# Kernel optimization log

Hardware: AMD Instinct MI355X
Metric: run time of the kernel (lower is better)

The kernel has to match this reference:

```python
import jax, jax.numpy as jnp
import numpy as np

B, T, C, HS = 256, 256, 384, 64


def setup_inputs() -> dict:
    key = jax.random.key(0)
    k1, k2, k3, k4 = jax.random.split(key, 4)
    X = jax.random.normal(k1, (B, T, C), dtype=jnp.float32)
    Wq = jax.random.normal(k2, (C, HS), dtype=jnp.float32) * (C ** -0.5)
    Wk = jax.random.normal(k3, (C, HS), dtype=jnp.float32) * (C ** -0.5)
    Wv = jax.random.normal(k4, (C, HS), dtype=jnp.float32) * (C ** -0.5)
    return {"X": X, "Wq": Wq, "Wk": Wk, "Wv": Wv}


def reference(X, Wq, Wk, Wv):
    # Single causal self-attention head (dropout in eval mode / identity).
    num_channels = X.shape[-1]
    q = jnp.einsum('btc,ch->bth', X, Wq)  # [B,T,HS]
    k = jnp.einsum('btc,ch->bth', X, Wk)
    v = jnp.einsum('btc,ch->bth', X, Wv)
    # NOTE: original scales by embedding dim C**-0.5, not head_size**-0.5.
    scores = jnp.einsum('bqh,bkh->bqk', q, k) * (num_channels ** -0.5)  # [B,T,T]
    Tq = X.shape[1]
    causal = jnp.tril(jnp.ones((Tq, Tq), dtype=bool))
    scores = jnp.where(causal, scores, jnp.float32(-jnp.inf))
    weights = jax.nn.softmax(scores, axis=-1)
    return jnp.einsum('bqk,bkh->bqh', weights, v)  # [B,T,HS]
```

## Files before the change

kernel.cpp:

```cpp
#include <hip/hip_runtime.h>
#include <hip/hip_bf16.h>

#define B_  256
#define T_  256
#define C_  384
#define HS_ 64
#define BT_ (B_*T_)

typedef __attribute__((ext_vector_type(8))) short short8;
typedef __attribute__((ext_vector_type(4))) float f32x4;

__device__ __forceinline__ unsigned short f2bf(float f) {
    unsigned u = __float_as_uint(f);
    u += 0x7FFFu + ((u >> 16) & 1u);
    return (unsigned short)(u >> 16);
}

__global__ __launch_bounds__(256) void prep_wfrag(
    const float* __restrict__ Wq, const float* __restrict__ Wk,
    const float* __restrict__ Wv, unsigned short* __restrict__ Wfrag)
{
    const int tid  = blockIdx.x * 256 + threadIdx.x;
    const int lane = tid & 63;
    const int q    = tid >> 6;
    const int f    = q % 3;
    const int q2   = q / 3;
    const int wn   = q2 & 3;
    const int s    = q2 >> 2;

    const int n     = wn * 48 + f * 16 + (lane & 15);
    const int kbase = s * 32 + (lane >> 4) * 8;
    const float* src = (n < 64) ? Wq : (n < 128) ? Wk : Wv;
    const int c      = n & 63;
    const float scale = (n < 64) ? 0.05103103630798288f : 1.0f;

    short8 out;
    #pragma unroll
    for (int j = 0; j < 8; ++j)
        out[j] = (short)f2bf(src[(size_t)(kbase + j) * HS_ + c] * scale);
    *(short8*)&Wfrag[(size_t)tid * 8] = out;
}

#define LQ_OFF 0
#define LK_OFF 18432
#define LV_OFF 36864
#define LX_OFF 53760

__global__ __launch_bounds__(1024, 4) void head_fused(
    const float* __restrict__ X, const unsigned short* __restrict__ Wfrag,
    float* __restrict__ out)
{
    __shared__ unsigned short lds[74240];
    const int t    = threadIdx.x;
    const int w    = t >> 6;
    const int lane = t & 63;
    const int lo   = lane & 15;
    const int hi   = lane >> 4;
    const int b    = blockIdx.x;
    const int wm   = w >> 2, wn = w & 3;

    const float* Xb = X + (size_t)b * T_ * C_;
    const short8* Wf = (const short8*)Wfrag;

    const int srow  = t >> 2;
    const int squad = t & 3;

    auto stage_load = [&](int k0, float4* g) {
        const float* p = Xb + (size_t)srow * C_ + k0 + squad * 8;
        g[0] = *(const float4*)(p);
        g[1] = *(const float4*)(p + 4);
    };
    auto stage_write = [&](int buf, const float4* g) {
        short8 p;
        p[0] = (short)f2bf(g[0].x); p[1] = (short)f2bf(g[0].y);
        p[2] = (short)f2bf(g[0].z); p[3] = (short)f2bf(g[0].w);
        p[4] = (short)f2bf(g[1].x); p[5] = (short)f2bf(g[1].y);
        p[6] = (short)f2bf(g[1].z); p[7] = (short)f2bf(g[1].w);
        *(short8*)&lds[LX_OFF + buf * 10240 + srow * 40 + squad * 8] = p;
    };
    auto load_w = [&](int s, short8* wf) {
        const short8* base = Wf + ((size_t)(s * 4 + wn) * 3) * 64 + lane;
        #pragma unroll
        for (int f = 0; f < 3; ++f)
            wf[f] = base[f * 64];
    };

    float4 gx[2][2];
    short8 wfr[2][3];
    stage_load(0, gx[0]);
    load_w(0, wfr[0]);
    stage_load(32, gx[1]);
    stage_write(0, gx[0]);
    __syncthreads();

    f32x4 acc[4][3];
    #pragma unroll
    for (int m = 0; m < 4; ++m)
        #pragma unroll
        for (int f = 0; f < 3; ++f)
            acc[m][f] = (f32x4){0.f, 0.f, 0.f, 0.f};

    #pragma unroll 2
    for (int s = 0; s < 12; ++s) {
        const int cur = s & 1;
        if (s < 10) stage_load((s + 2) * 32, gx[cur]);
        if (s < 11) load_w(s + 1, wfr[cur ^ 1]);
        if (s < 11) stage_write(cur ^ 1, gx[cur ^ 1]);

        short8 af[4];
        #pragma unroll
        for (int m = 0; m < 4; ++m)
            af[m] = *(const short8*)&lds[LX_OFF + cur * 10240 + (wm * 64 + m * 16 + lo) * 40 + hi * 8];
        #pragma unroll
        for (int m = 0; m < 4; ++m)
            #pragma unroll
            for (int f = 0; f < 3; ++f)
                acc[m][f] = __builtin_amdgcn_mfma_f32_16x16x32_bf16(af[m], wfr[cur][f], acc[m][f], 0, 0, 0);
        __syncthreads();
    }

    #pragma unroll
    for (int m = 0; m < 4; ++m) {
        const int rowb = wm * 64 + m * 16 + hi * 4;
        #pragma unroll
        for (int f = 0; f < 3; ++f) {
            const int base = wn * 48 + f * 16;
            if (base < 64) {
                #pragma unroll
                for (int r = 0; r < 4; ++r)
                    lds[LQ_OFF + (rowb + r) * 72 + base + lo] = f2bf(acc[m][f][r]);
            } else if (base < 128) {
                #pragma unroll
                for (int r = 0; r < 4; ++r)
                    lds[LK_OFF + (rowb + r) * 72 + (base - 64) + lo] = f2bf(acc[m][f][r]);
            } else {
                ushort4 pk = { f2bf(acc[m][f][0]), f2bf(acc[m][f][1]),
                               f2bf(acc[m][f][2]), f2bf(acc[m][f][3]) };
                *(ushort4*)&lds[LV_OFF + (base - 128 + lo) * 264 + rowb] = pk;
            }
        }
    }
    __syncthreads();

    const int sg  = w & 3, pos = w >> 2;
    const int tq  = (pos == 0) ? sg : (pos == 1) ? 15 - sg : (pos == 2) ? 4 + sg : 11 - sg;

    {
        const int q_lane = tq * 16 + lo;
        short8 qf0 = *(const short8*)&lds[LQ_OFF + q_lane * 72 + hi * 8];
        short8 qf1 = *(const short8*)&lds[LQ_OFF + q_lane * 72 + hi * 8 + 32];

        f32x4 acc_o[4];
        #pragma unroll
        for (int n = 0; n < 4; ++n) acc_o[n] = (f32x4){0.f, 0.f, 0.f, 0.f};
        float Mr = -1e30f, Lr = 0.f;

        const int nsteps = (tq >> 1) + 1;
        for (int s = 0; s < nsteps; ++s) {
            const int kv0 = s * 32;
            f32x4 sb[2];
            sb[0] = (f32x4){0.f, 0.f, 0.f, 0.f};
            sb[1] = (f32x4){0.f, 0.f, 0.f, 0.f};
            __builtin_amdgcn_s_setprio(1);
            #pragma unroll
            for (int n = 0; n < 2; ++n) {
                const unsigned short* kb = &lds[LK_OFF + (kv0 + n * 16 + lo) * 72 + hi * 8];
                short8 kf0 = *(const short8*)kb;
                short8 kf1 = *(const short8*)(kb + 32);
                sb[n] = __builtin_amdgcn_mfma_f32_16x16x32_bf16(kf0, qf0, sb[n], 0, 0, 0);
                sb[n] = __builtin_amdgcn_mfma_f32_16x16x32_bf16(kf1, qf1, sb[n], 0, 0, 0);
            }
            __builtin_amdgcn_s_setprio(0);
            if (s == nsteps - 1) {
                #pragma unroll
                for (int n = 0; n < 2; ++n)
                    #pragma unroll
                    for (int r = 0; r < 4; ++r)
                        if (kv0 + n * 16 + hi * 4 + r > q_lane) sb[n][r] = -1e30f;
            }
            float pmax = fmaxf(fmaxf(fmaxf(sb[0][0], sb[0][1]), fmaxf(sb[0][2], sb[0][3])),
                               fmaxf(fmaxf(sb[1][0], sb[1][1]), fmaxf(sb[1][2], sb[1][3])));
            pmax = fmaxf(pmax, __shfl_xor(pmax, 16));
            pmax = fmaxf(pmax, __shfl_xor(pmax, 32));
            float Mn;
            if (__all(pmax - Mr <= 8.0f)) {
                Mn = Mr;
            } else {
                Mn = fmaxf(Mr, pmax);
                const float fr = __expf(Mr - Mn);
                Mr = Mn;
                Lr *= fr;
                #pragma unroll
                for (int n = 0; n < 4; ++n) {
                    acc_o[n][0] *= fr; acc_o[n][1] *= fr;
                    acc_o[n][2] *= fr; acc_o[n][3] *= fr;
                }
            }
            float p0 = __expf(sb[0][0] - Mn), p1 = __expf(sb[0][1] - Mn);
            float p2 = __expf(sb[0][2] - Mn), p3 = __expf(sb[0][3] - Mn);
            float p4 = __expf(sb[1][0] - Mn), p5 = __expf(sb[1][1] - Mn);
            float p6 = __expf(sb[1][2] - Mn), p7 = __expf(sb[1][3] - Mn);
            float ls = ((p0 + p1) + (p2 + p3)) + ((p4 + p5) + (p6 + p7));
            ls += __shfl_xor(ls, 16);
            ls += __shfl_xor(ls, 32);
            Lr += ls;
            unsigned Ap, Bp, Cp, Dp;
            asm("v_cvt_pk_bf16_f32 %0, %1, %2" : "=v"(Ap) : "v"(p0), "v"(p1));
            asm("v_cvt_pk_bf16_f32 %0, %1, %2" : "=v"(Bp) : "v"(p2), "v"(p3));
            asm("v_cvt_pk_bf16_f32 %0, %1, %2" : "=v"(Cp) : "v"(p4), "v"(p5));
            asm("v_cvt_pk_bf16_f32 %0, %1, %2" : "=v"(Dp) : "v"(p6), "v"(p7));
            asm("v_permlane32_swap_b32 %0, %1" : "+v"(Ap), "+v"(Cp));
            asm("v_permlane16_swap_b32 %0, %1" : "+v"(Ap), "+v"(Cp));
            asm("v_permlane32_swap_b32 %0, %1" : "+v"(Bp), "+v"(Dp));
            asm("v_permlane16_swap_b32 %0, %1" : "+v"(Bp), "+v"(Dp));
            uint4 pfu = { Ap, Bp, Cp, Dp };
            short8 pf = *(short8*)&pfu;
            __builtin_amdgcn_s_setprio(1);
            #pragma unroll
            for (int n = 0; n < 4; ++n) {
                short8 vf = *(const short8*)&lds[LV_OFF + (n * 16 + lo) * 264 + kv0 + hi * 8];
                acc_o[n] = __builtin_amdgcn_mfma_f32_16x16x32_bf16(vf, pf, acc_o[n], 0, 0, 0);
            }
            __builtin_amdgcn_s_setprio(0);
        }
        const float inv = 1.0f / Lr;
        float* op = out + ((size_t)(b * 256 + q_lane)) * HS_;
        #pragma unroll
        for (int n = 0; n < 4; ++n)
            #pragma unroll
            for (int r = 0; r < 4; ++r)
                op[n * 16 + hi * 4 + r] = acc_o[n][r] * inv;
    }
}

extern "C" void kernel_launch(void* const* d_in, const int* in_sizes, int n_in,
                              void* d_out, int out_size, void* d_ws, size_t ws_size,
                              hipStream_t stream) {
    const float* X  = (const float*)d_in[0];
    const float* Wq = (const float*)d_in[1];
    const float* Wk = (const float*)d_in[2];
    const float* Wv = (const float*)d_in[3];
    float* out = (float*)d_out;

    unsigned short* Wfrag = (unsigned short*)d_ws;

    prep_wfrag<<<36, 256, 0, stream>>>(Wq, Wk, Wv, Wfrag);
    head_fused<<<B_, 1024, 0, stream>>>(X, Wfrag, out);
}
```

Baseline: 36.12 us.

## Split each batch across two blocks with global QKV exchange and flag sync

```diff
diff --git a/kernel.cpp b/kernel.cpp
--- a/kernel.cpp
+++ b/kernel.cpp
@@ -14,6 +14,10 @@
     unsigned u = __float_as_uint(f);
     u += 0x7FFFu + ((u >> 16) & 1u);
     return (unsigned short)(u >> 16);
+}
+
+__global__ __launch_bounds__(256) void zero_flags(int* __restrict__ flags) {
+    flags[threadIdx.x] = 0;
 }
 
 __global__ __launch_bounds__(256) void prep_wfrag(
@@ -41,25 +45,25 @@
     *(short8*)&Wfrag[(size_t)tid * 8] = out;
 }
 
-#define LQ_OFF 0
-#define LK_OFF 18432
-#define LV_OFF 36864
-#define LX_OFF 53760
-
-__global__ __launch_bounds__(1024, 4) void head_fused(
+__global__ __launch_bounds__(512, 4) void head_pc(
     const float* __restrict__ X, const unsigned short* __restrict__ Wfrag,
+    unsigned short* __restrict__ Qg, unsigned short* __restrict__ Kg,
+    unsigned short* __restrict__ Vtg, int* __restrict__ flags,
     float* __restrict__ out)
 {
-    __shared__ unsigned short lds[74240];
+    __shared__ unsigned short Xs[2][128 * 40];
     const int t    = threadIdx.x;
     const int w    = t >> 6;
     const int lane = t & 63;
     const int lo   = lane & 15;
     const int hi   = lane >> 4;
-    const int b    = blockIdx.x;
+    const int blk  = blockIdx.x;
+    const int b    = blk >> 1;
+    const int half = blk & 1;
     const int wm   = w >> 2, wn = w & 3;
 
-    const float* Xb = X + (size_t)b * T_ * C_;
+    const int row0 = b * 256 + half * 128;
+    const float* Xb = X + (size_t)row0 * C_;
     const short8* Wf = (const short8*)Wfrag;
 
     const int srow  = t >> 2;
@@ -71,12 +75,13 @@
         g[1] = *(const float4*)(p + 4);
     };
     auto stage_write = [&](int buf, const float4* g) {
-        short8 p;
-        p[0] = (short)f2bf(g[0].x); p[1] = (short)f2bf(g[0].y);
-        p[2] = (short)f2bf(g[0].z); p[3] = (short)f2bf(g[0].w);
-        p[4] = (short)f2bf(g[1].x); p[5] = (short)f2bf(g[1].y);
-        p[6] = (short)f2bf(g[1].z); p[7] = (short)f2bf(g[1].w);
-        *(short8*)&lds[LX_OFF + buf * 10240 + srow * 40 + squad * 8] = p;
+        unsigned a0, a1, a2, a3;
+        asm("v_cvt_pk_bf16_f32 %0, %1, %2" : "=v"(a0) : "v"(g[0].x), "v"(g[0].y));
+        asm("v_cvt_pk_bf16_f32 %0, %1, %2" : "=v"(a1) : "v"(g[0].z), "v"(g[0].w));
+        asm("v_cvt_pk_bf16_f32 %0, %1, %2" : "=v"(a2) : "v"(g[1].x), "v"(g[1].y));
+        asm("v_cvt_pk_bf16_f32 %0, %1, %2" : "=v"(a3) : "v"(g[1].z), "v"(g[1].w));
+        uint4 p = { a0, a1, a2, a3 };
+        *(uint4*)&Xs[buf][srow * 40 + squad * 8] = p;
     };
     auto load_w = [&](int s, short8* wf) {
         const short8* base = Wf + ((size_t)(s * 4 + wn) * 3) * 64 + lane;
@@ -110,7 +115,7 @@
         short8 af[4];
         #pragma unroll
         for (int m = 0; m < 4; ++m)
-            af[m] = *(const short8*)&lds[LX_OFF + cur * 10240 + (wm * 64 + m * 16 + lo) * 40 + hi * 8];
+            af[m] = *(const short8*)&Xs[cur][(wm * 64 + m * 16 + lo) * 40 + hi * 8];
         #pragma unroll
         for (int m = 0; m < 4; ++m)
             #pragma unroll
@@ -121,42 +126,54 @@
 
     #pragma unroll
     for (int m = 0; m < 4; ++m) {
-        const int rowb = wm * 64 + m * 16 + hi * 4;
+        const int grow = row0 + wm * 64 + m * 16 + hi * 4;
         #pragma unroll
         for (int f = 0; f < 3; ++f) {
             const int base = wn * 48 + f * 16;
+            const int n    = base + lo;
             if (base < 64) {
                 #pragma unroll
                 for (int r = 0; r < 4; ++r)
-                    lds[LQ_OFF + (rowb + r) * 72 + base + lo] = f2bf(acc[m][f][r]);
+                    Qg[(size_t)(grow + r) * HS_ + n] = f2bf(acc[m][f][r]);
             } else if (base < 128) {
                 #pragma unroll
                 for (int r = 0; r < 4; ++r)
-                    lds[LK_OFF + (rowb + r) * 72 + (base - 64) + lo] = f2bf(acc[m][f][r]);
+                    Kg[(size_t)(grow + r) * HS_ + (n - 64)] = f2bf(acc[m][f][r]);
             } else {
-                ushort4 pk = { f2bf(acc[m][f][0]), f2bf(acc[m][f][1]),
-                               f2bf(acc[m][f][2]), f2bf(acc[m][f][3]) };
-                *(ushort4*)&lds[LV_OFF + (base - 128 + lo) * 264 + rowb] = pk;
+                unsigned e0, e1;
+                asm("v_cvt_pk_bf16_f32 %0, %1, %2" : "=v"(e0) : "v"(acc[m][f][0]), "v"(acc[m][f][1]));
+                asm("v_cvt_pk_bf16_f32 %0, %1, %2" : "=v"(e1) : "v"(acc[m][f][2]), "v"(acc[m][f][3]));
+                uint2 pk = { e0, e1 };
+                *(uint2*)&Vtg[((size_t)(grow >> 8) * 64 + (n - 128)) * 256 + (grow & 255)] = pk;
             }
         }
     }
+
     __syncthreads();
-
-    const int sg  = w & 3, pos = w >> 2;
-    const int tq  = (pos == 0) ? sg : (pos == 1) ? 15 - sg : (pos == 2) ? 4 + sg : 11 - sg;
+    if (t == 0) {
+        __threadfence();
+        __hip_atomic_fetch_add(&flags[b], 1, __ATOMIC_RELEASE, __HIP_MEMORY_SCOPE_AGENT);
+        while (__hip_atomic_load(&flags[b], __ATOMIC_ACQUIRE, __HIP_MEMORY_SCOPE_AGENT) < 2)
+            __builtin_amdgcn_s_sleep(2);
+    }
+    __syncthreads();
 
     {
+        const int s_w = (w < 4) ? (w + 1) : (12 - w);
+        const int tq  = 2 * (s_w - 1) + half;
+        const int bb  = b * 256;
         const int q_lane = tq * 16 + lo;
-        short8 qf0 = *(const short8*)&lds[LQ_OFF + q_lane * 72 + hi * 8];
-        short8 qf1 = *(const short8*)&lds[LQ_OFF + q_lane * 72 + hi * 8 + 32];
+
+        const unsigned short* qp = Qg + ((size_t)(bb + q_lane)) * HS_ + hi * 8;
+        short8 qf0 = *(const short8*)qp;
+        short8 qf1 = *(const short8*)(qp + 32);
 
         f32x4 acc_o[4];
         #pragma unroll
         for (int n = 0; n < 4; ++n) acc_o[n] = (f32x4){0.f, 0.f, 0.f, 0.f};
         float Mr = -1e30f, Lr = 0.f;
 
-        const int nsteps = (tq >> 1) + 1;
-        for (int s = 0; s < nsteps; ++s) {
+        for (int s = 0; s < s_w; ++s) {
             const int kv0 = s * 32;
             f32x4 sb[2];
             sb[0] = (f32x4){0.f, 0.f, 0.f, 0.f};
@@ -164,14 +181,14 @@
             __builtin_amdgcn_s_setprio(1);
             #pragma unroll
             for (int n = 0; n < 2; ++n) {
-                const unsigned short* kb = &lds[LK_OFF + (kv0 + n * 16 + lo) * 72 + hi * 8];
+                const unsigned short* kb = Kg + ((size_t)(bb + kv0 + n * 16 + lo)) * HS_ + hi * 8;
                 short8 kf0 = *(const short8*)kb;
                 short8 kf1 = *(const short8*)(kb + 32);
                 sb[n] = __builtin_amdgcn_mfma_f32_16x16x32_bf16(kf0, qf0, sb[n], 0, 0, 0);
                 sb[n] = __builtin_amdgcn_mfma_f32_16x16x32_bf16(kf1, qf1, sb[n], 0, 0, 0);
             }
             __builtin_amdgcn_s_setprio(0);
-            if (s == nsteps - 1) {
+            if (s == s_w - 1) {
                 #pragma unroll
                 for (int n = 0; n < 2; ++n)
                     #pragma unroll
@@ -218,13 +235,14 @@
             __builtin_amdgcn_s_setprio(1);
             #pragma unroll
             for (int n = 0; n < 4; ++n) {
-                short8 vf = *(const short8*)&lds[LV_OFF + (n * 16 + lo) * 264 + kv0 + hi * 8];
+                const unsigned short* vb = Vtg + ((size_t)(b * 64 + n * 16 + lo)) * 256 + kv0 + hi * 8;
+                short8 vf = *(const short8*)vb;
                 acc_o[n] = __builtin_amdgcn_mfma_f32_16x16x32_bf16(vf, pf, acc_o[n], 0, 0, 0);
             }
             __builtin_amdgcn_s_setprio(0);
         }
         const float inv = 1.0f / Lr;
-        float* op = out + ((size_t)(b * 256 + q_lane)) * HS_;
+        float* op = out + ((size_t)(bb + q_lane)) * HS_;
         #pragma unroll
         for (int n = 0; n < 4; ++n)
             #pragma unroll
@@ -243,7 +261,12 @@
     float* out = (float*)d_out;
 
     unsigned short* Wfrag = (unsigned short*)d_ws;
-
+    unsigned short* Qg    = Wfrag + (size_t)9216 * 8;
+    unsigned short* Kg    = Qg + (size_t)BT_ * HS_;
+    unsigned short* Vtg   = Kg + (size_t)BT_ * HS_;
+    int*            flags = (int*)(Vtg + (size_t)BT_ * HS_);
+
+    zero_flags<<<1, 256, 0, stream>>>(flags);
     prep_wfrag<<<36, 256, 0, stream>>>(Wq, Wk, Wv, Wfrag);
-    head_fused<<<B_, 1024, 0, stream>>>(X, Wfrag, out);
-}
+    head_pc<<<512, 512, 0, stream>>>(X, Wfrag, Qg, Kg, Vtg, flags, out);
+}
```

Result: slower. 95.16 us (+163.5%).

## Load X fragments directly from global into MFMA registers, dropping LDS staging

Applied to the files above, without the earlier changes.

```diff
diff --git a/kernel.cpp b/kernel.cpp
--- a/kernel.cpp
+++ b/kernel.cpp
@@ -44,13 +44,12 @@
 #define LQ_OFF 0
 #define LK_OFF 18432
 #define LV_OFF 36864
-#define LX_OFF 53760
 
 __global__ __launch_bounds__(1024, 4) void head_fused(
     const float* __restrict__ X, const unsigned short* __restrict__ Wfrag,
     float* __restrict__ out)
 {
-    __shared__ unsigned short lds[74240];
+    __shared__ unsigned short lds[53760];
     const int t    = threadIdx.x;
     const int w    = t >> 6;
     const int lane = t & 63;
@@ -62,37 +61,6 @@
     const float* Xb = X + (size_t)b * T_ * C_;
     const short8* Wf = (const short8*)Wfrag;
 
-    const int srow  = t >> 2;
-    const int squad = t & 3;
-
-    auto stage_load = [&](int k0, float4* g) {
-        const float* p = Xb + (size_t)srow * C_ + k0 + squad * 8;
-        g[0] = *(const float4*)(p);
-        g[1] = *(const float4*)(p + 4);
-    };
-    auto stage_write = [&](int buf, const float4* g) {
-        short8 p;
-        p[0] = (short)f2bf(g[0].x); p[1] = (short)f2bf(g[0].y);
-        p[2] = (short)f2bf(g[0].z); p[3] = (short)f2bf(g[0].w);
-        p[4] = (short)f2bf(g[1].x); p[5] = (short)f2bf(g[1].y);
-        p[6] = (short)f2bf(g[1].z); p[7] = (short)f2bf(g[1].w);
-        *(short8*)&lds[LX_OFF + buf * 10240 + srow * 40 + squad * 8] = p;
-    };
-    auto load_w = [&](int s, short8* wf) {
-        const short8* base = Wf + ((size_t)(s * 4 + wn) * 3) * 64 + lane;
-        #pragma unroll
-        for (int f = 0; f < 3; ++f)
-            wf[f] = base[f * 64];
-    };
-
-    float4 gx[2][2];
-    short8 wfr[2][3];
-    stage_load(0, gx[0]);
-    load_w(0, wfr[0]);
-    stage_load(32, gx[1]);
-    stage_write(0, gx[0]);
-    __syncthreads();
-
     f32x4 acc[4][3];
     #pragma unroll
     for (int m = 0; m < 4; ++m)
@@ -102,21 +70,31 @@
 
     #pragma unroll 2
     for (int s = 0; s < 12; ++s) {
-        const int cur = s & 1;
-        if (s < 10) stage_load((s + 2) * 32, gx[cur]);
-        if (s < 11) load_w(s + 1, wfr[cur ^ 1]);
-        if (s < 11) stage_write(cur ^ 1, gx[cur ^ 1]);
-
+        const int k0 = s * 32;
+        short8 wf[3];
+        {
+            const short8* base = Wf + ((size_t)(s * 4 + wn) * 3) * 64 + lane;
+            wf[0] = base[0]; wf[1] = base[64]; wf[2] = base[128];
+        }
         short8 af[4];
         #pragma unroll
+        for (int m = 0; m < 4; ++m) {
+            const float* p = Xb + (size_t)(wm * 64 + m * 16 + lo) * C_ + k0 + hi * 8;
+            float4 a = *(const float4*)p;
+            float4 c = *(const float4*)(p + 4);
+            unsigned u0, u1, u2, u3;
+            asm("v_cvt_pk_bf16_f32 %0, %1, %2" : "=v"(u0) : "v"(a.x), "v"(a.y));
+            asm("v_cvt_pk_bf16_f32 %0, %1, %2" : "=v"(u1) : "v"(a.z), "v"(a.w));
+            asm("v_cvt_pk_bf16_f32 %0, %1, %2" : "=v"(u2) : "v"(c.x), "v"(c.y));
+            asm("v_cvt_pk_bf16_f32 %0, %1, %2" : "=v"(u3) : "v"(c.z), "v"(c.w));
+            uint4 pk = { u0, u1, u2, u3 };
+            af[m] = *(short8*)&pk;
+        }
+        #pragma unroll
         for (int m = 0; m < 4; ++m)
-            af[m] = *(const short8*)&lds[LX_OFF + cur * 10240 + (wm * 64 + m * 16 + lo) * 40 + hi * 8];
-        #pragma unroll
-        for (int m = 0; m < 4; ++m)
             #pragma unroll
             for (int f = 0; f < 3; ++f)
-                acc[m][f] = __builtin_amdgcn_mfma_f32_16x16x32_bf16(af[m], wfr[cur][f], acc[m][f], 0, 0, 0);
-        __syncthreads();
+                acc[m][f] = __builtin_amdgcn_mfma_f32_16x16x32_bf16(af[m], wf[f], acc[m][f], 0, 0, 0);
     }
 
     #pragma unroll
@@ -134,9 +112,11 @@
                 for (int r = 0; r < 4; ++r)
                     lds[LK_OFF + (rowb + r) * 72 + (base - 64) + lo] = f2bf(acc[m][f][r]);
             } else {
-                ushort4 pk = { f2bf(acc[m][f][0]), f2bf(acc[m][f][1]),
-                               f2bf(acc[m][f][2]), f2bf(acc[m][f][3]) };
-                *(ushort4*)&lds[LV_OFF + (base - 128 + lo) * 264 + rowb] = pk;
+                unsigned e0, e1;
+                asm("v_cvt_pk_bf16_f32 %0, %1, %2" : "=v"(e0) : "v"(acc[m][f][0]), "v"(acc[m][f][1]));
+                asm("v_cvt_pk_bf16_f32 %0, %1, %2" : "=v"(e1) : "v"(acc[m][f][2]), "v"(acc[m][f][3]));
+                uint2 pk = { e0, e1 };
+                *(uint2*)&lds[LV_OFF + (base - 128 + lo) * 264 + rowb] = pk;
             }
         }
     }
```

New measurement: 64.46 us. 78.5% more time.
